# Kernel tuning notes

Measured on AMD Instinct MI355X. Metric: run time of the kernel, lower is better.

The kernel has to match this reference:

```python
import jax, jax.numpy as jnp
import numpy as np

N = 100000   # nodes
E = 1600000  # edges
IN = 41      # in_channels (21 atom + 20 residue)
ED = 8       # edge_dim
H = 64       # hidden_dim
L = 3        # num_layers
G = 256      # graphs in batch
ATOM = 21
EPS = 1e-5   # GraphNorm eps


def setup_inputs() -> dict:
    key = jax.random.key(0)
    ks = jax.random.split(key, 32)
    s = 0.1
    x = jax.random.normal(ks[0], (N, IN), jnp.float32)
    # make even-index nodes 'ligand' atoms (zero residue part) so both MLP branches fire
    lig = (jnp.arange(N) % 2) == 0
    x = x.at[:, ATOM:].set(jnp.where(lig[:, None], 0.0, x[:, ATOM:]))
    edge_index = jax.random.randint(ks[1], (2, E), 0, N)
    edge_attr = jax.random.normal(ks[2], (E, ED), jnp.float32)
    batch = jnp.sort(jax.random.randint(ks[3], (N,), 0, G))
    p = {
        "lig_W1": s * jax.random.normal(ks[4], (IN, H), jnp.float32),
        "lig_b1": jnp.zeros((H,), jnp.float32),
        "lig_W2": s * jax.random.normal(ks[5], (H, H), jnp.float32),
        "lig_b2": jnp.zeros((H,), jnp.float32),
        "prot_W1": s * jax.random.normal(ks[6], (IN, H), jnp.float32),
        "prot_b1": jnp.zeros((H,), jnp.float32),
        "prot_W2": s * jax.random.normal(ks[7], (H, H), jnp.float32),
        "prot_b2": jnp.zeros((H,), jnp.float32),
        # per-layer stacked params for the 3 GINEConv + GraphNorm blocks
        "conv_We": s * jax.random.normal(ks[8], (L, ED, H), jnp.float32),
        "conv_be": jnp.zeros((L, H), jnp.float32),
        "conv_W1": s * jax.random.normal(ks[9], (L, H, H), jnp.float32),
        "conv_b1": jnp.zeros((L, H), jnp.float32),
        "conv_W2": s * jax.random.normal(ks[10], (L, H, H), jnp.float32),
        "conv_b2": jnp.zeros((L, H), jnp.float32),
        "norm_w": jnp.ones((L, H), jnp.float32),
        "norm_b": jnp.zeros((L, H), jnp.float32),
        "norm_a": jnp.ones((L, H), jnp.float32),  # mean_scale alpha
        "out_W1": s * jax.random.normal(ks[11], (H, H), jnp.float32),
        "out_b1": jnp.zeros((H,), jnp.float32),
        "out_W2": s * jax.random.normal(ks[12], (H, 1), jnp.float32),
        "out_b2": jnp.zeros((1,), jnp.float32),
    }
    return dict(x=x, edge_index=edge_index, edge_attr=edge_attr, batch=batch, **p)


def reference(x, edge_index, edge_attr, batch,
              lig_W1, lig_b1, lig_W2, lig_b2,
              prot_W1, prot_b1, prot_W2, prot_b2,
              conv_We, conv_be, conv_W1, conv_b1, conv_W2, conv_b2,
              norm_w, norm_b, norm_a,
              out_W1, out_b1, out_W2, out_b2):
    # --- input encoder: ligand vs protein branch by residue-part mask ---
    res_mask = jnp.sum(jnp.abs(x[:, ATOM:]), axis=1) > 1e-6
    h_lig = jax.nn.relu(jax.nn.relu(x @ lig_W1 + lig_b1) @ lig_W2 + lig_b2)
    h_prot = jax.nn.relu(jax.nn.relu(x @ prot_W1 + prot_b1) @ prot_W2 + prot_b2)
    h = jnp.where(res_mask[:, None], h_prot, h_lig)  # [N, H]

    src, dst = edge_index[0], edge_index[1]
    counts = jnp.maximum(jax.ops.segment_sum(jnp.ones((N,), h.dtype), batch,
                                             num_segments=G), 1.0)[:, None]  # [G,1]

    for l in range(L):
        # GINEConv (eps=0): nn(h_i + sum_j relu(h_j + lin(e_ij)))
        e = edge_attr @ conv_We[l] + conv_be[l]           # [E, H]
        msg = jax.nn.relu(h[src] + e)                     # [E, H]
        aggr = jax.ops.segment_sum(msg, dst, num_segments=N)
        z = h + aggr
        h = jax.nn.relu(z @ conv_W1[l] + conv_b1[l]) @ conv_W2[l] + conv_b2[l]
        # GraphNorm: (h - alpha*mean_g) / sqrt(var_g + eps) * w + b
        mean = jax.ops.segment_sum(h, batch, num_segments=G) / counts  # [G, H]
        out = h - norm_a[l] * mean[batch]
        var = jax.ops.segment_sum(out * out, batch, num_segments=G) / counts
        h = norm_w[l] * (out / jnp.sqrt(var + EPS)[batch]) + norm_b[l]
        h = jax.nn.relu(h)

    # global_add_pool + readout (dropout = identity at eval)
    g = jax.ops.segment_sum(h, batch, num_segments=G)  # [G, H]
    out = jax.nn.relu(g @ out_W1 + out_b1) @ out_W2 + out_b2  # [G, 1]
    return out.reshape(-1)
```

## Files before the change

kernel.cpp:

```cpp
#include <hip/hip_runtime.h>

#define NN 100000
#define NE 1600000
#define IN_CH 41
#define EDIM 8
#define H 64
#define GNUM 256
#define ATOM 21
#define EPSV 1e-5f
#define EPW 16
#define NTILE (NN / 16)

#define BSH2 3
#define BDST2 8
#define NBK2 12500
#define VPT 8
#define EPB_H (1024 * VPT)
#define NBLK_H ((NE + EPB_H - 1) / EPB_H)

typedef unsigned short u16;
typedef unsigned int u32;
typedef unsigned long long u64;
typedef __attribute__((ext_vector_type(8))) short short8;
typedef __attribute__((ext_vector_type(4))) float floatx4;

__device__ __forceinline__ u16 f2bf(float f) {
    u32 u = __float_as_uint(f);
    u32 r = (u + 0x7FFFu + ((u >> 16) & 1u)) >> 16;
    return (u16)r;
}
__device__ __forceinline__ float bf2f(u16 u) {
    return __uint_as_float(((u32)u) << 16);
}
__device__ __forceinline__ floatx4 mfma16(short8 a, short8 b, floatx4 c) {
    return __builtin_amdgcn_mfma_f32_16x16x32_bf16(a, b, c, 0, 0, 0);
}
__device__ __forceinline__ short8 pack_bf8(float4 a, float4 b) {
    short8 s;
    s[0] = (short)f2bf(a.x); s[1] = (short)f2bf(a.y);
    s[2] = (short)f2bf(a.z); s[3] = (short)f2bf(a.w);
    s[4] = (short)f2bf(b.x); s[5] = (short)f2bf(b.y);
    s[6] = (short)f2bf(b.z); s[7] = (short)f2bf(b.w);
    return s;
}

__global__ __launch_bounds__(256) void partition_kernel(
    const float* __restrict__ x, int* __restrict__ ctr,
    int* __restrict__ lig_list, int* __restrict__ prot_list)
{
    const int n = blockIdx.x * 256 + threadIdx.x;
    const int lane = threadIdx.x & 63;
    float m = 0.0f;
    if (n < NN) {
        const float* xr = x + (size_t)n * IN_CH + ATOM;
#pragma unroll
        for (int d = 0; d < IN_CH - ATOM; ++d) m += fabsf(xr[d]);
    }
    const bool valid = n < NN;
    const bool prot = valid && (m > 1e-6f);
    const bool lig = valid && !prot;

    const u64 bl = __ballot(lig);
    const u64 bp = __ballot(prot);
    const u64 below_m = (lane == 63) ? (~0ull >> 1) : ((1ull << lane) - 1ull);
    int base_l = 0, base_p = 0;
    if (lane == 0) {
        if (bl) base_l = atomicAdd(&ctr[0], (int)__popcll(bl));
        if (bp) base_p = atomicAdd(&ctr[1], (int)__popcll(bp));
    }
    base_l = __shfl(base_l, 0, 64);
    base_p = __shfl(base_p, 0, 64);
    if (lig)  lig_list [base_l + (int)__popcll(bl & below_m)] = n;
    if (prot) prot_list[base_p + (int)__popcll(bp & below_m)] = n;
}

__global__ __launch_bounds__(256) void xb_kernel(
    const float* __restrict__ x, u16* __restrict__ xb)
{
    const int id = blockIdx.x * 256 + threadIdx.x;
    if (id >= NN * H) return;
    const int n = id >> 6, d = id & 63;
    xb[id] = (d < IN_CH) ? f2bf(x[(size_t)n * IN_CH + d]) : (u16)0;
}

__global__ __launch_bounds__(256) void ea2b_kernel(
    const float* __restrict__ ea, uint4* __restrict__ eab16g)
{
    const int e = blockIdx.x * 256 + threadIdx.x;
    if (e >= NE) return;
    const float4* e4 = (const float4*)(ea + (size_t)e * EDIM);
    const float4 a = e4[0], b = e4[1];
    uint4 u;
    u.x = (u32)f2bf(a.x) | ((u32)f2bf(a.y) << 16);
    u.y = (u32)f2bf(a.z) | ((u32)f2bf(a.w) << 16);
    u.z = (u32)f2bf(b.x) | ((u32)f2bf(b.y) << 16);
    u.w = (u32)f2bf(b.z) | ((u32)f2bf(b.w) << 16);
    eab16g[e] = u;
}

__global__ __launch_bounds__(256) void prep_w_kernel(
    const float* __restrict__ ligW1, const float* __restrict__ ligW2,
    const float* __restrict__ protW1, const float* __restrict__ protW2,
    const float* __restrict__ convW1, const float* __restrict__ convW2,
    u16* __restrict__ wf)
{
    const int id = blockIdx.x * 256 + threadIdx.x;
    if (id >= 10 * 4096) return;
    const int j = id & 7, l = (id >> 3) & 63, t = (id >> 9) & 3;
    const int c = (id >> 11) & 1, mat = id >> 12;
    const int k = c * 32 + ((l >> 4) * 8) + j;
    const int n = t * 16 + (l & 15);
    const float* src; int K = 64;
    if (mat == 0)      { src = ligW1;  K = IN_CH; }
    else if (mat == 1) { src = ligW2; }
    else if (mat == 2) { src = protW1; K = IN_CH; }
    else if (mat == 3) { src = protW2; }
    else {
        const int layer = (mat - 4) >> 1;
        src = (((mat - 4) & 1) ? convW2 : convW1) + (size_t)layer * H * H;
    }
    wf[id] = (k < K) ? f2bf(src[(size_t)k * H + n]) : (u16)0;
}

__global__ __launch_bounds__(256) void enc_mfma_kernel(
    const int* __restrict__ list, const int* __restrict__ countPtr,
    const u16* __restrict__ xb,
    const u16* __restrict__ w1f, const u16* __restrict__ w2f,
    const float* __restrict__ bia1, const float* __restrict__ bia2,
    float* __restrict__ h, u16* __restrict__ h16)
{
    __shared__ __align__(16) u16 hid[4][16 * 72];
    const int wv = threadIdx.x >> 6;
    const int lane = threadIdx.x & 63;
    const int tile = blockIdx.x * 4 + wv;
    const int count = *countPtr;
    if (tile * 16 >= count) return;
    const int quad = lane >> 4;
    const int mi = lane & 15;
    int idx = tile * 16 + mi;
    if (idx >= count) idx = count - 1;
    const int nid = list[idx];

    const short8 a0 = *(const short8*)(xb + (size_t)nid * H + quad * 8);
    const short8 a1 = *(const short8*)(xb + (size_t)nid * H + 32 + quad * 8);

    floatx4 acc[4];
#pragma unroll
    for (int t = 0; t < 4; ++t) acc[t] = (floatx4){0.f, 0.f, 0.f, 0.f};
#pragma unroll
    for (int t = 0; t < 4; ++t) {
        const short8 b0 = *(const short8*)(w1f + ((size_t)(0 * 4 + t) * 64 + lane) * 8);
        const short8 b1 = *(const short8*)(w1f + ((size_t)(1 * 4 + t) * 64 + lane) * 8);
        acc[t] = mfma16(a0, b0, acc[t]);
        acc[t] = mfma16(a1, b1, acc[t]);
    }

    u16* myh = hid[wv];
#pragma unroll
    for (int t = 0; t < 4; ++t) {
        const float bv = bia1[t * 16 + mi];
#pragma unroll
        for (int r = 0; r < 4; ++r) {
            const float v = fmaxf(acc[t][r] + bv, 0.0f);
            myh[(quad * 4 + r) * 72 + t * 16 + mi] = f2bf(v);
        }
    }
    asm volatile("s_waitcnt lgkmcnt(0)" ::: "memory");

    const short8 c0 = *(const short8*)(myh + mi * 72 + quad * 8);
    const short8 c1 = *(const short8*)(myh + mi * 72 + 32 + quad * 8);

    floatx4 acc2[4];
#pragma unroll
    for (int t = 0; t < 4; ++t) acc2[t] = (floatx4){0.f, 0.f, 0.f, 0.f};
#pragma unroll
    for (int t = 0; t < 4; ++t) {
        const short8 b0 = *(const short8*)(w2f + ((size_t)(0 * 4 + t) * 64 + lane) * 8);
        const short8 b1 = *(const short8*)(w2f + ((size_t)(1 * 4 + t) * 64 + lane) * 8);
        acc2[t] = mfma16(c0, b0, acc2[t]);
        acc2[t] = mfma16(c1, b1, acc2[t]);
    }

#pragma unroll
    for (int t = 0; t < 4; ++t) {
        const float bv = bia2[t * 16 + mi];
#pragma unroll
        for (int r = 0; r < 4; ++r) {
            const int row = quad * 4 + r;
            const int nr = __shfl(nid, row, 64);
            if (tile * 16 + row < count) {
                const float v = fmaxf(acc2[t][r] + bv, 0.0f);
                h[(size_t)nr * H + t * 16 + mi] = v;
                h16[(size_t)nr * H + t * 16 + mi] = f2bf(v);
            }
        }
    }
}

__global__ __launch_bounds__(256) void mlp_mfma_kernel(
    const u16* __restrict__ w1f, const u16* __restrict__ w2f,
    const float* __restrict__ bia1, const float* __restrict__ bia2,
    float* __restrict__ h)
{
    __shared__ __align__(16) u16 hid[4][16 * 72];
    const int wv = threadIdx.x >> 6;
    const int lane = threadIdx.x & 63;
    const int tile = blockIdx.x * 4 + wv;
    if (tile >= NTILE) return;
    const int quad = lane >> 4;
    const int mi = lane & 15;
    const int row = tile * 16 + mi;
    const float* zr = h + (size_t)row * H;

    const float4 f0 = *(const float4*)(zr + quad * 8);
    const float4 f1 = *(const float4*)(zr + quad * 8 + 4);
    const float4 f2 = *(const float4*)(zr + 32 + quad * 8);
    const float4 f3 = *(const float4*)(zr + 32 + quad * 8 + 4);
    const short8 a0 = pack_bf8(f0, f1);
    const short8 a1 = pack_bf8(f2, f3);

    floatx4 acc[4];
#pragma unroll
    for (int t = 0; t < 4; ++t) acc[t] = (floatx4){0.f, 0.f, 0.f, 0.f};
#pragma unroll
    for (int t = 0; t < 4; ++t) {
        const short8 b0 = *(const short8*)(w1f + ((size_t)(0 * 4 + t) * 64 + lane) * 8);
        const short8 b1 = *(const short8*)(w1f + ((size_t)(1 * 4 + t) * 64 + lane) * 8);
        acc[t] = mfma16(a0, b0, acc[t]);
        acc[t] = mfma16(a1, b1, acc[t]);
    }

    u16* myh = hid[wv];
#pragma unroll
    for (int t = 0; t < 4; ++t) {
        const float bv = bia1[t * 16 + mi];
#pragma unroll
        for (int r = 0; r < 4; ++r) {
            const float v = fmaxf(acc[t][r] + bv, 0.0f);
            myh[(quad * 4 + r) * 72 + t * 16 + mi] = f2bf(v);
        }
    }
    asm volatile("s_waitcnt lgkmcnt(0)" ::: "memory");

    const short8 c0 = *(const short8*)(myh + mi * 72 + quad * 8);
    const short8 c1 = *(const short8*)(myh + mi * 72 + 32 + quad * 8);

    floatx4 acc2[4];
#pragma unroll
    for (int t = 0; t < 4; ++t) acc2[t] = (floatx4){0.f, 0.f, 0.f, 0.f};
#pragma unroll
    for (int t = 0; t < 4; ++t) {
        const short8 b0 = *(const short8*)(w2f + ((size_t)(0 * 4 + t) * 64 + lane) * 8);
        const short8 b1 = *(const short8*)(w2f + ((size_t)(1 * 4 + t) * 64 + lane) * 8);
        acc2[t] = mfma16(c0, b0, acc2[t]);
        acc2[t] = mfma16(c1, b1, acc2[t]);
    }

#pragma unroll
    for (int t = 0; t < 4; ++t) {
        const float bv = bia2[t * 16 + mi];
#pragma unroll
        for (int r = 0; r < 4; ++r) {
            const int orow = tile * 16 + quad * 4 + r;
            h[(size_t)orow * H + t * 16 + mi] = acc2[t][r] + bv;
        }
    }
}

__global__ void bounds_kernel(const int* __restrict__ batch, int* __restrict__ start)
{
    int g = blockIdx.x * blockDim.x + threadIdx.x;
    if (g > GNUM) return;
    int lo = 0, hi = NN;
    while (lo < hi) {
        int mid = (lo + hi) >> 1;
        if (batch[mid] < g) lo = mid + 1; else hi = mid;
    }
    start[g] = lo;
}

__global__ __launch_bounds__(1024) void bhist_kernel(
    const int* __restrict__ ei, int* __restrict__ gbcount)
{
    __shared__ int cnt[NBK2];
    const int t = threadIdx.x;
    for (int i = t; i < NBK2; i += 1024) cnt[i] = 0;
    __syncthreads();
    const int base = blockIdx.x * EPB_H;
#pragma unroll
    for (int v = 0; v < VPT; ++v) {
        const int e = base + v * 1024 + t;
        if (e < NE) atomicAdd(&cnt[ei[NE + e] >> BSH2], 1);
    }
    __syncthreads();
    for (int i = t; i < NBK2; i += 1024)
        if (cnt[i]) atomicAdd(&gbcount[i], cnt[i]);
}

__global__ __launch_bounds__(1024) void bscan_kernel(
    const int* __restrict__ gbcount, int* __restrict__ gstart, int* __restrict__ gcur)
{
    __shared__ int s[1024];
    __shared__ int carry_s;
    const int t = threadIdx.x;
    if (t == 0) carry_s = 0;
    __syncthreads();
    for (int tile = 0; tile * 1024 < NBK2; ++tile) {
        const int idx = tile * 1024 + t;
        const int v = (idx < NBK2) ? gbcount[idx] : 0;
        s[t] = v;
        __syncthreads();
#pragma unroll
        for (int off = 1; off < 1024; off <<= 1) {
            int tmp = (t >= off) ? s[t - off] : 0;
            __syncthreads();
            s[t] += tmp;
            __syncthreads();
        }
        const int carry = carry_s;
        if (idx < NBK2) {
            const int ex = carry + s[t] - v;
            gstart[idx] = ex;
            gcur[idx] = ex;
        }
        __syncthreads();
        if (t == 1023) carry_s = carry + s[1023];
        __syncthreads();
    }
    if (t == 0) gstart[NBK2] = NE;
}

__global__ __launch_bounds__(1024) void p1_kernel(
    const int* __restrict__ ei, const uint4* __restrict__ eab16g,
    int* __restrict__ gcur,
    u32* __restrict__ brec, uint4* __restrict__ bfeat)
{
    __shared__ int cnt[NBK2];
    const int t = threadIdx.x;
    for (int i = t; i < NBK2; i += 1024) cnt[i] = 0;
    __syncthreads();
    const int base = blockIdx.x * EPB_H;
    int dstv[VPT];
#pragma unroll
    for (int v = 0; v < VPT; ++v) {
        const int e = base + v * 1024 + t;
        dstv[v] = -1;
        if (e < NE) {
            dstv[v] = ei[NE + e];
            atomicAdd(&cnt[dstv[v] >> BSH2], 1);
        }
    }
    __syncthreads();
    for (int i = t; i < NBK2; i += 1024) {
        const int c = cnt[i];
        cnt[i] = c ? atomicAdd(&gcur[i], c) : 0;
    }
    __syncthreads();
#pragma unroll
    for (int v = 0; v < VPT; ++v) {
        const int e = base + v * 1024 + t;
        if (e < NE) {
            const int b = dstv[v] >> BSH2;
            const int pos = atomicAdd(&cnt[b], 1);
            brec[pos] = (u32)ei[e] | ((u32)(dstv[v] & (BDST2 - 1)) << 17);
            bfeat[pos] = eab16g[e];
        }
    }
}

__global__ __launch_bounds__(256) void aggr_kernel(
    const u32* __restrict__ brec,
    const u32* __restrict__ bfeat32,
    const int* __restrict__ gstart,
    const float* __restrict__ We, const float* __restrict__ be,
    const u16* __restrict__ h16, float* __restrict__ h)
{
    const int lane = threadIdx.x & 63;
    const int bk = blockIdx.x * 4 + (threadIdx.x >> 6);
    const int s = gstart[bk], e = gstart[bk + 1];

    float we_r[EDIM];
#pragma unroll
    for (int d = 0; d < EDIM; ++d) we_r[d] = We[d * H + lane];
    const float be_r = be[lane];

    float a0 = 0.f, a1 = 0.f, a2 = 0.f, a3 = 0.f;
    float a4 = 0.f, a5 = 0.f, a6 = 0.f, a7 = 0.f;

    for (int base = s; base < e; base += EPW) {
        const int cnt = min(EPW, e - base);
        u32 rec = 0;
        if ((lane & 15) < cnt) rec = brec[base + (lane & 15)];
        u32 eu = 0;
        if (lane < cnt * 4) eu = bfeat32[(size_t)base * 4 + lane];

        float hv[EPW];
#pragma unroll
        for (int j = 0; j < EPW; ++j) {
            const int sj = (int)(__builtin_amdgcn_readlane(rec, j) & 0x1ffffu);
            hv[j] = bf2f(h16[(size_t)sj * H + lane]);
        }
#pragma unroll
        for (int j = 0; j < EPW; ++j) {
            if (j < cnt) {
                const u32 rj = __builtin_amdgcn_readlane(rec, j);
                const int ld = (int)(rj >> 17);
                float msg = be_r;
#pragma unroll
                for (int p = 0; p < 4; ++p) {
                    const u32 w2 = __builtin_amdgcn_readlane(eu, j * 4 + p);
                    msg = fmaf(__uint_as_float(w2 << 16), we_r[2 * p], msg);
                    msg = fmaf(__uint_as_float(w2 & 0xffff0000u), we_r[2 * p + 1], msg);
                }
                const float val = fmaxf(hv[j] + msg, 0.0f);
                if (ld < 4) {
                    if (ld < 2) { if (ld == 0) a0 += val; else a1 += val; }
                    else        { if (ld == 2) a2 += val; else a3 += val; }
                } else {
                    if (ld < 6) { if (ld == 4) a4 += val; else a5 += val; }
                    else        { if (ld == 6) a6 += val; else a7 += val; }
                }
            }
        }
    }

    float* hr = h + (size_t)bk * BDST2 * H + lane;
    hr[0 * H] += a0; hr[1 * H] += a1; hr[2 * H] += a2; hr[3 * H] += a3;
    hr[4 * H] += a4; hr[5 * H] += a5; hr[6 * H] += a6; hr[7 * H] += a7;
}

__global__ __launch_bounds__(1024) void graphnorm_kernel(
    float* __restrict__ h, u16* __restrict__ h16,
    const int* __restrict__ start,
    const float* __restrict__ w, const float* __restrict__ b,
    const float* __restrict__ a,
    float* __restrict__ pool, int do_pool)
{
    __shared__ float red1[16][H], red2[16][H];
    __shared__ float amean_s[H], rstd_s[H];
    const int g = blockIdx.x;
    const int lane = threadIdx.x & 63;
    const int wv = threadIdx.x >> 6;
    const int s = start[g], e = start[g + 1];

    float s1 = 0.f, s2 = 0.f;
    for (int i = s + wv; i < e; i += 16) {
        float v = h[(size_t)i * H + lane];
        s1 += v; s2 += v * v;
    }
    red1[wv][lane] = s1; red2[wv][lane] = s2;
    __syncthreads();
    if (threadIdx.x < H) {
        float t1 = 0.f, t2 = 0.f;
#pragma unroll
        for (int k = 0; k < 16; ++k) { t1 += red1[k][lane]; t2 += red2[k][lane]; }
        float cnt = fmaxf((float)(e - s), 1.0f);
        float mean = t1 / cnt;
        float alpha = a[lane];
        float var = t2 / cnt - (2.0f * alpha - alpha * alpha) * mean * mean;
        var = fmaxf(var, 0.0f);
        amean_s[lane] = alpha * mean;
        rstd_s[lane] = rsqrtf(var + EPSV);
    }
    __syncthreads();
    const float am = amean_s[lane], rstd = rstd_s[lane];
    const float ww = w[lane], bb = b[lane];
    float ps = 0.f;
    for (int i = s + wv; i < e; i += 16) {
        float v = (h[(size_t)i * H + lane] - am) * rstd * ww + bb;
        v = fmaxf(v, 0.0f);
        h[(size_t)i * H + lane] = v;
        h16[(size_t)i * H + lane] = f2bf(v);
        ps += v;
    }
    if (do_pool && e > s) unsafeAtomicAdd(&pool[g * H + lane], ps);
}

__global__ __launch_bounds__(64) void final_kernel(
    const float* __restrict__ pool,
    const float* __restrict__ W1, const float* __restrict__ b1,
    const float* __restrict__ W2, const float* __restrict__ b2,
    float* __restrict__ out)
{
    const int g = blockIdx.x;
    const int lane = threadIdx.x;
    const float gv = pool[g * H + lane];
    float acc = b1[lane];
#pragma unroll
    for (int d = 0; d < H; ++d)
        acc = fmaf(__shfl(gv, d, 64), W1[d * H + lane], acc);
    float r = fmaxf(acc, 0.0f);
    float v = r * W2[lane];
#pragma unroll
    for (int o = 32; o > 0; o >>= 1) v += __shfl_xor(v, o, 64);
    if (lane == 0) out[g] = v + b2[0];
}

extern "C" void kernel_launch(void* const* d_in, const int* in_sizes, int n_in,
                              void* d_out, int out_size, void* d_ws, size_t ws_size,
                              hipStream_t stream)
{
    const float* x      = (const float*)d_in[0];
    const int*   ei     = (const int*)  d_in[1];
    const float* ea     = (const float*)d_in[2];
    const int*   batch  = (const int*)  d_in[3];
    const float* ligW1  = (const float*)d_in[4];
    const float* ligb1  = (const float*)d_in[5];
    const float* ligW2  = (const float*)d_in[6];
    const float* ligb2  = (const float*)d_in[7];
    const float* protW1 = (const float*)d_in[8];
    const float* protb1 = (const float*)d_in[9];
    const float* protW2 = (const float*)d_in[10];
    const float* protb2 = (const float*)d_in[11];
    const float* convWe = (const float*)d_in[12];
    const float* convbe = (const float*)d_in[13];
    const float* convW1 = (const float*)d_in[14];
    const float* convb1 = (const float*)d_in[15];
    const float* convW2 = (const float*)d_in[16];
    const float* convb2 = (const float*)d_in[17];
    const float* normw  = (const float*)d_in[18];
    const float* normb  = (const float*)d_in[19];
    const float* norma  = (const float*)d_in[20];
    const float* outW1  = (const float*)d_in[21];
    const float* outb1  = (const float*)d_in[22];
    const float* outW2  = (const float*)d_in[23];
    const float* outb2  = (const float*)d_in[24];

    float* out = (float*)d_out;

    float* h         = (float*)d_ws;
    uint4* bfeat     = (uint4*)(h + (size_t)NN * H);
    u32*   brec      = (u32*)(bfeat + (size_t)NE);
    u16*   h16       = (u16*)(brec + (size_t)NE);
    u16*   xb        = h16 + (size_t)NN * H;
    u16*   wf        = xb + (size_t)NN * H;
    uint4* eab16g    = (uint4*)h16;

    int*   ctr       = (int*)(wf + 40960);
    int*   gbcount   = ctr + 2;
    float* pool      = (float*)(gbcount + NBK2);
    int*   gstart    = (int*)(pool + GNUM * H);
    int*   gcur      = gstart + (NBK2 + 1);
    int*   start     = gcur + NBK2;
    int*   lig_list  = start + (GNUM + 1);
    int*   prot_list = lig_list + NN;

    hipMemsetAsync(ctr, 0, ((size_t)2 + NBK2 + GNUM * H) * sizeof(int), stream);

    prep_w_kernel<<<(10 * 4096 + 255) / 256, 256, 0, stream>>>(
        ligW1, ligW2, protW1, protW2, convW1, convW2, wf);
    partition_kernel<<<(NN + 255) / 256, 256, 0, stream>>>(x, ctr, lig_list, prot_list);
    bounds_kernel<<<2, 256, 0, stream>>>(batch, start);

    bhist_kernel<<<NBLK_H, 1024, 0, stream>>>(ei, gbcount);
    bscan_kernel<<<1, 1024, 0, stream>>>(gbcount, gstart, gcur);
    ea2b_kernel<<<(NE + 255) / 256, 256, 0, stream>>>(ea, eab16g);
    p1_kernel<<<NBLK_H, 1024, 0, stream>>>(ei, eab16g, gcur, brec, bfeat);

    xb_kernel<<<(NN * H + 255) / 256, 256, 0, stream>>>(x, xb);
    const int enc_blocks = (NTILE + 3) / 4;
    enc_mfma_kernel<<<enc_blocks, 256, 0, stream>>>(
        lig_list, &ctr[0], xb, wf + 0 * 4096, wf + 1 * 4096, ligb1, ligb2, h, h16);
    enc_mfma_kernel<<<enc_blocks, 256, 0, stream>>>(
        prot_list, &ctr[1], xb, wf + 2 * 4096, wf + 3 * 4096, protb1, protb2, h, h16);

    const int aggr_blocks = NBK2 / 4;
    const int mlp_blocks = (NTILE + 3) / 4;
    for (int l = 0; l < 3; ++l) {
        aggr_kernel<<<aggr_blocks, 256, 0, stream>>>(
            brec, (const u32*)bfeat, gstart,
            convWe + (size_t)l * EDIM * H, convbe + (size_t)l * H, h16, h);
        mlp_mfma_kernel<<<mlp_blocks, 256, 0, stream>>>(
            wf + (size_t)(4 + 2 * l) * 4096, wf + (size_t)(5 + 2 * l) * 4096,
            convb1 + (size_t)l * H, convb2 + (size_t)l * H, h);
        graphnorm_kernel<<<GNUM, 1024, 0, stream>>>(
            h, h16, start, normw + (size_t)l * H, normb + (size_t)l * H,
            norma + (size_t)l * H, pool, (l == 2) ? 1 : 0);
    }
    final_kernel<<<GNUM, 64, 0, stream>>>(pool, outW1, outb1, outW2, outb2, out);
}
```

Measured before the change: 733.9 us.

## Bucket edges by exact destination node with global atomic counting sort

Replaces the 8-node bucket histogram/scan/scatter built with shared-memory atomics by a per-node counting sort that uses global atomics, plus a two-kernel multi-block scan over all nodes. The aggregation kernel now walks edges sorted by destination and keeps a single running accumulator, flushing it to h with atomic adds whenever the destination changes, instead of eight branchy per-slot accumulators. This removes the long serial single-block scan and the branching in the aggregation loop. In exchange it adds heavy global atomic contention when sorting 1.6M edges, float atomics in aggr that make summation order nondeterministic, and a larger workspace.

Measured after the change: 736.4 us. About the same (+0.3%).

```diff
diff --git a/kernel.cpp b/kernel.cpp
--- a/kernel.cpp
+++ b/kernel.cpp
@@ -11,12 +11,9 @@
 #define EPW 16
 #define NTILE (NN / 16)
 
-#define BSH2 3
 #define BDST2 8
 #define NBK2 12500
-#define VPT 8
-#define EPB_H (1024 * VPT)
-#define NBLK_H ((NE + EPB_H - 1) / EPB_H)
+#define NBLK_S ((NN + 1023) / 1024)
 
 typedef unsigned short u16;
 typedef unsigned int u32;
@@ -279,96 +276,71 @@
     start[g] = lo;
 }
 
-__global__ __launch_bounds__(1024) void bhist_kernel(
+__global__ __launch_bounds__(256) void bhist_kernel(
     const int* __restrict__ ei, int* __restrict__ gbcount)
 {
-    __shared__ int cnt[NBK2];
+    const int e = blockIdx.x * 256 + threadIdx.x;
+    if (e < NE) atomicAdd(&gbcount[ei[NE + e]], 1);
+}
+
+__global__ __launch_bounds__(1024) void scanA_kernel(
+    const int* __restrict__ gbcount, int* __restrict__ gstart, int* __restrict__ gsums)
+{
+    __shared__ int s[1024];
     const int t = threadIdx.x;
-    for (int i = t; i < NBK2; i += 1024) cnt[i] = 0;
+    const int idx = blockIdx.x * 1024 + t;
+    const int v = (idx < NN) ? gbcount[idx] : 0;
+    s[t] = v;
     __syncthreads();
-    const int base = blockIdx.x * EPB_H;
-#pragma unroll
-    for (int v = 0; v < VPT; ++v) {
-        const int e = base + v * 1024 + t;
-        if (e < NE) atomicAdd(&cnt[ei[NE + e] >> BSH2], 1);
-    }
+#pragma unroll
+    for (int off = 1; off < 1024; off <<= 1) {
+        int tmp = (t >= off) ? s[t - off] : 0;
+        __syncthreads();
+        s[t] += tmp;
+        __syncthreads();
+    }
+    if (idx < NN) gstart[idx] = s[t] - v;
+    if (t == 1023) gsums[blockIdx.x] = s[1023];
+}
+
+__global__ __launch_bounds__(1024) void scanB_kernel(
+    int* __restrict__ gstart, int* __restrict__ gcur, const int* __restrict__ gsums)
+{
+    __shared__ int sm[128];
+    __shared__ int off_s;
+    const int t = threadIdx.x;
+    const int b = blockIdx.x;
+    if (t < NBLK_S) sm[t] = gsums[t];
     __syncthreads();
-    for (int i = t; i < NBK2; i += 1024)
-        if (cnt[i]) atomicAdd(&gbcount[i], cnt[i]);
-}
-
-__global__ __launch_bounds__(1024) void bscan_kernel(
-    const int* __restrict__ gbcount, int* __restrict__ gstart, int* __restrict__ gcur)
-{
-    __shared__ int s[1024];
-    __shared__ int carry_s;
-    const int t = threadIdx.x;
-    if (t == 0) carry_s = 0;
+    if (t == 0) {
+        int o = 0;
+        for (int i = 0; i < b; ++i) o += sm[i];
+        off_s = o;
+    }
     __syncthreads();
-    for (int tile = 0; tile * 1024 < NBK2; ++tile) {
-        const int idx = tile * 1024 + t;
-        const int v = (idx < NBK2) ? gbcount[idx] : 0;
-        s[t] = v;
-        __syncthreads();
-#pragma unroll
-        for (int off = 1; off < 1024; off <<= 1) {
-            int tmp = (t >= off) ? s[t - off] : 0;
-            __syncthreads();
-            s[t] += tmp;
-            __syncthreads();
-        }
-        const int carry = carry_s;
-        if (idx < NBK2) {
-            const int ex = carry + s[t] - v;
-            gstart[idx] = ex;
-            gcur[idx] = ex;
-        }
-        __syncthreads();
-        if (t == 1023) carry_s = carry + s[1023];
-        __syncthreads();
-    }
-    if (t == 0) gstart[NBK2] = NE;
-}
-
-__global__ __launch_bounds__(1024) void p1_kernel(
+    const int idx = b * 1024 + t;
+    if (idx < NN) {
+        const int g = gstart[idx] + off_s;
+        gstart[idx] = g;
+        gcur[idx] = g;
+    }
+    if (b == 0 && t == 0) gstart[NN] = NE;
+}
+
+__global__ __launch_bounds__(256) void p1_kernel(
     const int* __restrict__ ei, const uint4* __restrict__ eab16g,
     int* __restrict__ gcur,
     u32* __restrict__ brec, uint4* __restrict__ bfeat)
 {
-    __shared__ int cnt[NBK2];
-    const int t = threadIdx.x;
-    for (int i = t; i < NBK2; i += 1024) cnt[i] = 0;
-    __syncthreads();
-    const int base = blockIdx.x * EPB_H;
-    int dstv[VPT];
-#pragma unroll
-    for (int v = 0; v < VPT; ++v) {
-        const int e = base + v * 1024 + t;
-        dstv[v] = -1;
-        if (e < NE) {
-            dstv[v] = ei[NE + e];
-            atomicAdd(&cnt[dstv[v] >> BSH2], 1);
-        }
-    }
-    __syncthreads();
-    for (int i = t; i < NBK2; i += 1024) {
-        const int c = cnt[i];
-        cnt[i] = c ? atomicAdd(&gcur[i], c) : 0;
-    }
-    __syncthreads();
-#pragma unroll
-    for (int v = 0; v < VPT; ++v) {
-        const int e = base + v * 1024 + t;
-        if (e < NE) {
-            const int b = dstv[v] >> BSH2;
-            const int pos = atomicAdd(&cnt[b], 1);
-            brec[pos] = (u32)ei[e] | ((u32)(dstv[v] & (BDST2 - 1)) << 17);
-            bfeat[pos] = eab16g[e];
-        }
-    }
-}
-
-__global__ __launch_bounds__(256) void aggr_kernel(
+    const int e = blockIdx.x * 256 + threadIdx.x;
+    if (e >= NE) return;
+    const int dst = ei[NE + e];
+    const int pos = atomicAdd(&gcur[dst], 1);
+    brec[pos] = (u32)ei[e] | ((u32)(dst & (BDST2 - 1)) << 17);
+    bfeat[pos] = eab16g[e];
+}
+
+__global__ __launch_bounds__(256, 4) void aggr_kernel(
     const u32* __restrict__ brec,
     const u32* __restrict__ bfeat32,
     const int* __restrict__ gstart,
@@ -377,15 +349,17 @@
 {
     const int lane = threadIdx.x & 63;
     const int bk = blockIdx.x * 4 + (threadIdx.x >> 6);
-    const int s = gstart[bk], e = gstart[bk + 1];
+    const int row0 = bk * BDST2;
+    const int s = gstart[row0], e = gstart[row0 + BDST2];
+    if (s >= e) return;
 
     float we_r[EDIM];
 #pragma unroll
     for (int d = 0; d < EDIM; ++d) we_r[d] = We[d * H + lane];
     const float be_r = be[lane];
 
-    float a0 = 0.f, a1 = 0.f, a2 = 0.f, a3 = 0.f;
-    float a4 = 0.f, a5 = 0.f, a6 = 0.f, a7 = 0.f;
+    float acc = 0.0f;
+    int cur = -1;
 
     for (int base = s; base < e; base += EPW) {
         const int cnt = min(EPW, e - base);
@@ -413,20 +387,17 @@
                     msg = fmaf(__uint_as_float(w2 & 0xffff0000u), we_r[2 * p + 1], msg);
                 }
                 const float val = fmaxf(hv[j] + msg, 0.0f);
-                if (ld < 4) {
-                    if (ld < 2) { if (ld == 0) a0 += val; else a1 += val; }
-                    else        { if (ld == 2) a2 += val; else a3 += val; }
-                } else {
-                    if (ld < 6) { if (ld == 4) a4 += val; else a5 += val; }
-                    else        { if (ld == 6) a6 += val; else a7 += val; }
+                if (ld != cur) {
+                    if (cur >= 0)
+                        unsafeAtomicAdd(&h[(size_t)(row0 + cur) * H + lane], acc);
+                    acc = 0.0f;
+                    cur = ld;
                 }
+                acc += val;
             }
         }
     }
-
-    float* hr = h + (size_t)bk * BDST2 * H + lane;
-    hr[0 * H] += a0; hr[1 * H] += a1; hr[2 * H] += a2; hr[3 * H] += a3;
-    hr[4 * H] += a4; hr[5 * H] += a5; hr[6 * H] += a6; hr[7 * H] += a7;
+    unsafeAtomicAdd(&h[(size_t)(row0 + cur) * H + lane], acc);
 }
 
 __global__ __launch_bounds__(1024) void graphnorm_kernel(
@@ -538,24 +509,26 @@
 
     int*   ctr       = (int*)(wf + 40960);
     int*   gbcount   = ctr + 2;
-    float* pool      = (float*)(gbcount + NBK2);
+    float* pool      = (float*)(gbcount + NN);
     int*   gstart    = (int*)(pool + GNUM * H);
-    int*   gcur      = gstart + (NBK2 + 1);
-    int*   start     = gcur + NBK2;
+    int*   gcur      = gstart + (NN + 1);
+    int*   gsums     = gcur + NN;
+    int*   start     = gsums + 128;
     int*   lig_list  = start + (GNUM + 1);
     int*   prot_list = lig_list + NN;
 
-    hipMemsetAsync(ctr, 0, ((size_t)2 + NBK2 + GNUM * H) * sizeof(int), stream);
+    hipMemsetAsync(ctr, 0, ((size_t)2 + NN + GNUM * H) * sizeof(int), stream);
 
     prep_w_kernel<<<(10 * 4096 + 255) / 256, 256, 0, stream>>>(
         ligW1, ligW2, protW1, protW2, convW1, convW2, wf);
     partition_kernel<<<(NN + 255) / 256, 256, 0, stream>>>(x, ctr, lig_list, prot_list);
     bounds_kernel<<<2, 256, 0, stream>>>(batch, start);
 
-    bhist_kernel<<<NBLK_H, 1024, 0, stream>>>(ei, gbcount);
-    bscan_kernel<<<1, 1024, 0, stream>>>(gbcount, gstart, gcur);
+    bhist_kernel<<<NE / 256, 256, 0, stream>>>(ei, gbcount);
+    scanA_kernel<<<NBLK_S, 1024, 0, stream>>>(gbcount, gstart, gsums);
+    scanB_kernel<<<NBLK_S, 1024, 0, stream>>>(gstart, gcur, gsums);
     ea2b_kernel<<<(NE + 255) / 256, 256, 0, stream>>>(ea, eab16g);
-    p1_kernel<<<NBLK_H, 1024, 0, stream>>>(ei, eab16g, gcur, brec, bfeat);
+    p1_kernel<<<NE / 256, 256, 0, stream>>>(ei, eab16g, gcur, brec, bfeat);
 
     xb_kernel<<<(NN * H + 255) / 256, 256, 0, stream>>>(x, xb);
     const int enc_blocks = (NTILE + 3) / 4;
```
